# Optimization experiments

Measured on AMD Instinct MI355X. Metric: run time of the kernel, lower is better.

The kernel has to match this reference:

```python
import jax, jax.numpy as jnp
import numpy as np

N, V, E_PER = 8, 4608, 73728          # batch, nodes per graph, edges per graph
D_IN, C, NCLS = 1, 512, 3             # node feat dim, embed dim, classes
E = N * E_PER
LN_EPS = 1e-5


def setup_inputs() -> dict:
    key = jax.random.key(0)
    ks = jax.random.split(key, 12)
    x = jax.random.normal(ks[0], (N, 1, V, D_IN), jnp.float32)
    edge_index = jax.random.randint(ks[1], (2, E), 0, V, dtype=jnp.int32)
    edge_weight = jax.random.uniform(ks[2], (E,), jnp.float32)
    # GCNConv params: layer0 maps D_IN->C, layers 1..2 map C->C (weight [in,out], bias [out])
    w0 = jax.random.normal(ks[3], (D_IN, C), jnp.float32) * 0.02
    b0 = jnp.zeros((C,), jnp.float32)
    w1 = jax.random.normal(ks[4], (C, C), jnp.float32) * 0.02
    b1 = jnp.zeros((C,), jnp.float32)
    w2 = jax.random.normal(ks[5], (C, C), jnp.float32) * 0.02
    b2 = jnp.zeros((C,), jnp.float32)
    ln_g = jnp.ones((C,), jnp.float32)
    ln_b = jnp.zeros((C,), jnp.float32)
    head_w = jax.random.normal(ks[6], (C, NCLS), jnp.float32) * 2e-5
    head_b = jnp.log(jnp.full((NCLS,), 1.0 / NCLS, jnp.float32))
    return {"x": x, "edge_weight": edge_weight, "w0": w0, "b0": b0,
            "w1": w1, "b1": b1, "w2": w2, "b2": b2,
            "ln_g": ln_g, "ln_b": ln_b, "head_w": head_w, "head_b": head_b,
            "edge_index": edge_index}


def layer_norm(h, g, b):
    mu = h.mean(-1, keepdims=True)
    var = ((h - mu) ** 2).mean(-1, keepdims=True)
    return (h - mu) * jax.lax.rsqrt(var + LN_EPS) * g + b


def reference(x, edge_weight, w0, b0, w1, b1, w2, b2, ln_g, ln_b, head_w, head_b, edge_index):
    n, t, v, d = x.shape
    nv = n * v
    h = x.reshape(nv, d)
    # batch-offset local edge indices (edges are contiguous per graph)
    offs = jnp.repeat(jnp.arange(n, dtype=edge_index.dtype) * v, edge_index.shape[1] // n)
    src = edge_index[0] + offs
    tgt = edge_index[1] + offs
    # GCN norm with self-loops (fill weight 1.0), symmetric deg^-1/2 normalization
    loop = jnp.arange(nv, dtype=src.dtype)
    src_f = jnp.concatenate([src, loop])
    tgt_f = jnp.concatenate([tgt, loop])
    ew_f = jnp.concatenate([edge_weight, jnp.ones((nv,), edge_weight.dtype)])
    deg = jax.ops.segment_sum(ew_f, tgt_f, num_segments=nv)
    deg_safe = jnp.where(deg > 0, deg, 1.0)
    dinv = jnp.where(deg > 0, jax.lax.rsqrt(deg_safe), 0.0)
    norm = dinv[src_f] * ew_f * dinv[tgt_f]
    for w, bb in ((w0, b0), (w1, b1), (w2, b2)):
        hw = h @ w                                   # [NV, C]
        msg = norm[:, None] * hw[src_f]              # gather + scale  [E+NV, C]
        h = jax.ops.segment_sum(msg, tgt_f, num_segments=nv) + bb
        h = jax.nn.relu(h)
        h = layer_norm(h, ln_g, ln_b)
        # dropout is identity in eval mode
    pooled = h.reshape(n, v, -1).max(axis=1)         # global_max_pool (contiguous batch)
    pooled = layer_norm(pooled, ln_g, ln_b)
    return pooled @ head_w + head_b                  # [N, NCLS]
```

## Files before the change

### kernel.cpp

```cpp
#include <hip/hip_runtime.h>
#include <hip/hip_bf16.h>
#include <stdint.h>

#define N_GRAPH 8
#define V_NODES 4608
#define E_PER   73728
#define NV      (N_GRAPH * V_NODES)
#define E_TOT   (N_GRAPH * E_PER)
#define C       512
#define NCLS    3
#define LN_EPS  1e-5f
#define POOL_CHUNKS 36
#define SCAN_BLOCKS 144

typedef __attribute__((ext_vector_type(8))) short short8;
typedef __attribute__((ext_vector_type(4))) float floatx4;
typedef __attribute__((address_space(1))) void v_g;
typedef __attribute__((address_space(3))) void v_l;


__device__ inline float waveReduceSum(float v) {
#pragma unroll
    for (int o = 32; o > 0; o >>= 1) v += __shfl_down(v, o, 64);
    return v;
}

__device__ inline float waveAllSum(float v) {
#pragma unroll
    for (int o = 32; o > 0; o >>= 1) v += __shfl_xor(v, o, 64);
    return v;
}

__device__ inline float blockSum512(float v, volatile float* sred) {
    float s = waveReduceSum(v);
    if ((threadIdx.x & 63) == 0) sred[threadIdx.x >> 6] = s;
    __syncthreads();
    float t = 0.f;
#pragma unroll
    for (int i = 0; i < 8; i++) t += sred[i];
    __syncthreads();
    return t;
}

__device__ inline unsigned short f2bf(float f) {
    uint32_t u = __float_as_uint(f);
    u += 0x7fffu + ((u >> 16) & 1u);
    return (unsigned short)(u >> 16);
}
__device__ inline float bf2f(unsigned short b) {
    return __uint_as_float(((uint32_t)b) << 16);
}


__global__ void k_init(float* dinv, int* counts) {
    int i = blockIdx.x * 256 + threadIdx.x;
    if (i < NV) { dinv[i] = 1.0f; counts[i] = 0; }
}

__global__ void k_deg_count(const int* __restrict__ ei, const float* __restrict__ ew,
                            float* __restrict__ dinv, int* __restrict__ counts) {
    int e = blockIdx.x * 256 + threadIdx.x;
    if (e >= E_TOT) return;
    int off = (e / E_PER) * V_NODES;
    int t = ei[E_TOT + e] + off;
    atomicAdd(&dinv[t], ew[e]);
    atomicAdd(&counts[t], 1);
}

__global__ void k_rsqrt(float* dinv) {
    int i = blockIdx.x * 256 + threadIdx.x;
    if (i < NV) dinv[i] = rsqrtf(dinv[i]);
}


__global__ void k_scan1(const int* __restrict__ counts, int* __restrict__ row_ptr,
                        int* __restrict__ bsum) {
    __shared__ int sh[256];
    const int b = blockIdx.x, tid = threadIdx.x;
    const int idx = b * 256 + tid;
    int v = counts[idx];
    sh[tid] = v;
    __syncthreads();
#pragma unroll
    for (int off = 1; off < 256; off <<= 1) {
        int t = (tid >= off) ? sh[tid - off] : 0;
        __syncthreads();
        sh[tid] += t;
        __syncthreads();
    }
    row_ptr[idx] = sh[tid] - v;
    if (tid == 255) bsum[b] = sh[255];
}

__global__ void k_scan2(int* __restrict__ bsum) {
    __shared__ int sh[256];
    const int tid = threadIdx.x;
    int v = (tid < SCAN_BLOCKS) ? bsum[tid] : 0;
    sh[tid] = v;
    __syncthreads();
#pragma unroll
    for (int off = 1; off < 256; off <<= 1) {
        int t = (tid >= off) ? sh[tid - off] : 0;
        __syncthreads();
        sh[tid] += t;
        __syncthreads();
    }
    if (tid < SCAN_BLOCKS) bsum[tid] = sh[tid] - v;
}

__global__ void k_scan3(int* __restrict__ row_ptr, const int* __restrict__ bsum,
                        int* __restrict__ cursor) {
    const int b = blockIdx.x, tid = threadIdx.x;
    const int idx = b * 256 + tid;
    int v = row_ptr[idx] + bsum[b];
    row_ptr[idx] = v;
    cursor[idx] = v;
    if (idx == 0) row_ptr[NV] = E_TOT;
}

__global__ void k_fill(const int* __restrict__ ei, const float* __restrict__ ew,
                       const float* __restrict__ dinv, int* __restrict__ cursor,
                       int* __restrict__ col_idx, float* __restrict__ val) {
    int e = blockIdx.x * 256 + threadIdx.x;
    if (e >= E_TOT) return;
    int off = (e / E_PER) * V_NODES;
    int s = ei[e] + off;
    int t = ei[E_TOT + e] + off;
    int pos = atomicAdd(&cursor[t], 1);
    col_idx[pos] = s;
    val[pos] = dinv[s] * ew[e] * dinv[t];
}


__global__ void k_wt(const float* __restrict__ w1, const float* __restrict__ w2,
                     unsigned short* __restrict__ wt1, unsigned short* __restrict__ wt2) {
    int idx = blockIdx.x * 256 + threadIdx.x;
    int which = idx >> 18;
    int rem = idx & 0x3ffff;
    int n = rem >> 9, k = rem & 511;
    const float* W = which ? w2 : w1;
    unsigned short* WT = which ? wt2 : wt1;
    WT[n * C + k] = f2bf(W[k * C + n]);
}


__global__ void k_agg0_scalar(const float* __restrict__ x, const int* __restrict__ row_ptr,
                              const int* __restrict__ col_idx, const float* __restrict__ val,
                              const float* __restrict__ dinv, float* __restrict__ s0) {
    int t = blockIdx.x * 256 + threadIdx.x;
    if (t >= NV) return;
    float dt = dinv[t];
    float acc = dt * dt * x[t];
    int e1 = row_ptr[t + 1];
    for (int e = row_ptr[t]; e < e1; e++)
        acc += val[e] * x[col_idx[e]];
    s0[t] = acc;
}

__launch_bounds__(128)
__global__ void k_l0post(const float* __restrict__ s0, const float* __restrict__ w0,
                         const float* __restrict__ b0, const float* __restrict__ ln_g,
                         const float* __restrict__ ln_b, unsigned short* __restrict__ out) {
    const int t = blockIdx.x;
    const int tid = threadIdx.x;
    const int c4 = tid << 2;
    float s = s0[t];
    float4 w = *reinterpret_cast<const float4*>(&w0[c4]);
    float4 bb = *reinterpret_cast<const float4*>(&b0[c4]);
    float vx = fmaxf(s * w.x + bb.x, 0.f);
    float vy = fmaxf(s * w.y + bb.y, 0.f);
    float vz = fmaxf(s * w.z + bb.z, 0.f);
    float vw = fmaxf(s * w.w + bb.w, 0.f);
    __shared__ float redA[2], redB[2];
    float wsum = waveReduceSum(vx + vy + vz + vw);
    if ((tid & 63) == 0) redA[tid >> 6] = wsum;
    __syncthreads();
    float mu = (redA[0] + redA[1]) * (1.0f / C);
    float dx = vx - mu, dy = vy - mu, dz = vz - mu, dw = vw - mu;
    float wsq = waveReduceSum(dx * dx + dy * dy + dz * dz + dw * dw);
    if ((tid & 63) == 0) redB[tid >> 6] = wsq;
    __syncthreads();
    float rstd = rsqrtf((redB[0] + redB[1]) * (1.0f / C) + LN_EPS);
    float4 g = *reinterpret_cast<const float4*>(&ln_g[c4]);
    float4 b = *reinterpret_cast<const float4*>(&ln_b[c4]);
    ushort4 o = { f2bf(dx * rstd * g.x + b.x), f2bf(dy * rstd * g.y + b.y),
                  f2bf(dz * rstd * g.z + b.z), f2bf(dw * rstd * g.w + b.w) };
    reinterpret_cast<ushort4*>(out)[(size_t)t * 128 + tid] = o;
}


__launch_bounds__(256)
__global__ void k_gemm_mfma(const unsigned short* __restrict__ A,
                            const unsigned short* __restrict__ WT,
                            unsigned short* __restrict__ Bout) {
    __shared__ short8 lA[512];
    __shared__ short8 lB[512];
    const int tid = threadIdx.x;
    const int lane = tid & 63;
    const int wave = tid >> 6;
    const int wr = wave >> 1, wc = wave & 1;
    const int l15 = lane & 15, kg = lane >> 4;
    const int m0 = blockIdx.x * 128;
    const int n0 = blockIdx.y * 128;

    floatx4 acc[4][4] = {};

    const int s0i = tid, s1i = 256 + tid;
    const int kgs0 = s0i >> 7, idx0 = s0i & 127;
    const int kgs1 = s1i >> 7, idx1 = s1i & 127;
    const unsigned short* gA0 = A + (size_t)(m0 + idx0) * C + kgs0 * 8;
    const unsigned short* gA1 = A + (size_t)(m0 + idx1) * C + kgs1 * 8;
    const unsigned short* gB0 = WT + (size_t)(n0 + idx0) * C + kgs0 * 8;
    const unsigned short* gB1 = WT + (size_t)(n0 + idx1) * C + kgs1 * 8;

    for (int k0 = 0; k0 < C; k0 += 32) {
        __builtin_amdgcn_global_load_lds((v_g*)(gA0 + k0), (v_l*)&lA[s0i], 16, 0, 0);
        __builtin_amdgcn_global_load_lds((v_g*)(gA1 + k0), (v_l*)&lA[s1i], 16, 0, 0);
        __builtin_amdgcn_global_load_lds((v_g*)(gB0 + k0), (v_l*)&lB[s0i], 16, 0, 0);
        __builtin_amdgcn_global_load_lds((v_g*)(gB1 + k0), (v_l*)&lB[s1i], 16, 0, 0);
        asm volatile("s_waitcnt vmcnt(0)" ::: "memory");
        __syncthreads();

        short8 af[4], bf[4];
#pragma unroll
        for (int mi = 0; mi < 4; mi++)
            af[mi] = lA[kg * 128 + wr * 64 + mi * 16 + l15];
#pragma unroll
        for (int ni = 0; ni < 4; ni++)
            bf[ni] = lB[kg * 128 + wc * 64 + ni * 16 + l15];
#pragma unroll
        for (int mi = 0; mi < 4; mi++)
#pragma unroll
            for (int ni = 0; ni < 4; ni++)
                acc[mi][ni] = __builtin_amdgcn_mfma_f32_16x16x32_bf16(
                    af[mi], bf[ni], acc[mi][ni], 0, 0, 0);
        __syncthreads();
    }

#pragma unroll
    for (int mi = 0; mi < 4; mi++) {
#pragma unroll
        for (int ni = 0; ni < 4; ni++) {
            int n = n0 + wc * 64 + ni * 16 + l15;
#pragma unroll
            for (int r = 0; r < 4; r++) {
                int m = m0 + wr * 64 + mi * 16 + kg * 4 + r;
                Bout[(size_t)m * C + n] = f2bf(acc[mi][ni][r]);
            }
        }
    }
}


__launch_bounds__(256)
__global__ void k_agg(const unsigned short* __restrict__ hw, const int* __restrict__ row_ptr,
                      const int* __restrict__ col_idx, const float* __restrict__ val,
                      const float* __restrict__ dinv, const float* __restrict__ bias,
                      const float* __restrict__ ln_g, const float* __restrict__ ln_b,
                      unsigned short* __restrict__ out) {
    const int b = blockIdx.x;
    const int wv = threadIdx.x >> 6;
    const int lane = threadIdx.x & 63;
    const int t = (b & 7) * V_NODES + ((b >> 3) << 2) + wv;
    const int e0 = row_ptr[t], e1 = row_ptr[t + 1];
    const short8* hw8 = reinterpret_cast<const short8*>(hw);

    const float dt = dinv[t];
    const float selfw = dt * dt;
    short8 hs = hw8[(size_t)t * 64 + lane];
    float a[8];
#pragma unroll
    for (int i = 0; i < 8; i++) a[i] = selfw * bf2f((unsigned short)hs[i]);

    int e = e0;
    for (; e + 4 <= e1; e += 4) {
        int i0 = col_idx[e], i1 = col_idx[e + 1], i2 = col_idx[e + 2], i3 = col_idx[e + 3];
        float w0 = val[e], w1 = val[e + 1], w2 = val[e + 2], w3 = val[e + 3];
        short8 h0 = hw8[(size_t)i0 * 64 + lane];
        short8 h1 = hw8[(size_t)i1 * 64 + lane];
        short8 h2 = hw8[(size_t)i2 * 64 + lane];
        short8 h3 = hw8[(size_t)i3 * 64 + lane];
#pragma unroll
        for (int i = 0; i < 8; i++) a[i] += w0 * bf2f((unsigned short)h0[i]);
#pragma unroll
        for (int i = 0; i < 8; i++) a[i] += w1 * bf2f((unsigned short)h1[i]);
#pragma unroll
        for (int i = 0; i < 8; i++) a[i] += w2 * bf2f((unsigned short)h2[i]);
#pragma unroll
        for (int i = 0; i < 8; i++) a[i] += w3 * bf2f((unsigned short)h3[i]);
    }
    for (; e < e1; e++) {
        int is = col_idx[e];
        float w = val[e];
        short8 hv = hw8[(size_t)is * 64 + lane];
#pragma unroll
        for (int i = 0; i < 8; i++) a[i] += w * bf2f((unsigned short)hv[i]);
    }

    const int c8 = lane << 3;
    float4 bb0 = *reinterpret_cast<const float4*>(&bias[c8]);
    float4 bb1 = *reinterpret_cast<const float4*>(&bias[c8 + 4]);
    a[0] = fmaxf(a[0] + bb0.x, 0.f); a[1] = fmaxf(a[1] + bb0.y, 0.f);
    a[2] = fmaxf(a[2] + bb0.z, 0.f); a[3] = fmaxf(a[3] + bb0.w, 0.f);
    a[4] = fmaxf(a[4] + bb1.x, 0.f); a[5] = fmaxf(a[5] + bb1.y, 0.f);
    a[6] = fmaxf(a[6] + bb1.z, 0.f); a[7] = fmaxf(a[7] + bb1.w, 0.f);

    float s = a[0] + a[1] + a[2] + a[3] + a[4] + a[5] + a[6] + a[7];
    float mu = waveAllSum(s) * (1.0f / C);
    float sq = 0.f;
#pragma unroll
    for (int i = 0; i < 8; i++) { float d = a[i] - mu; sq += d * d; }
    float rstd = rsqrtf(waveAllSum(sq) * (1.0f / C) + LN_EPS);

    float4 g0 = *reinterpret_cast<const float4*>(&ln_g[c8]);
    float4 g1 = *reinterpret_cast<const float4*>(&ln_g[c8 + 4]);
    float4 z0 = *reinterpret_cast<const float4*>(&ln_b[c8]);
    float4 z1 = *reinterpret_cast<const float4*>(&ln_b[c8 + 4]);
    short8 o;
    o[0] = (short)f2bf((a[0] - mu) * rstd * g0.x + z0.x);
    o[1] = (short)f2bf((a[1] - mu) * rstd * g0.y + z0.y);
    o[2] = (short)f2bf((a[2] - mu) * rstd * g0.z + z0.z);
    o[3] = (short)f2bf((a[3] - mu) * rstd * g0.w + z0.w);
    o[4] = (short)f2bf((a[4] - mu) * rstd * g1.x + z1.x);
    o[5] = (short)f2bf((a[5] - mu) * rstd * g1.y + z1.y);
    o[6] = (short)f2bf((a[6] - mu) * rstd * g1.z + z1.z);
    o[7] = (short)f2bf((a[7] - mu) * rstd * g1.w + z1.w);
    reinterpret_cast<short8*>(out)[(size_t)t * 64 + lane] = o;
}


__global__ void k_pool1(const unsigned short* __restrict__ h, float* __restrict__ pmax) {
    int g = blockIdx.x, chunk = blockIdx.y;
    int c = threadIdx.x;
    int r0 = g * V_NODES + chunk * 128;
    float m = -1e30f;
#pragma unroll 4
    for (int r = 0; r < 128; r++)
        m = fmaxf(m, bf2f(h[(size_t)(r0 + r) * C + c]));
    pmax[((size_t)g * POOL_CHUNKS + chunk) * C + c] = m;
}

__global__ void k_pool2_head(const float* __restrict__ pmax, const float* __restrict__ ln_g,
                             const float* __restrict__ ln_b, const float* __restrict__ hw,
                             const float* __restrict__ hb, float* __restrict__ out) {
    __shared__ float sred[8];
    int g = blockIdx.x;
    int c = threadIdx.x;
    float m = -1e30f;
#pragma unroll
    for (int j = 0; j < POOL_CHUNKS; j++)
        m = fmaxf(m, pmax[((size_t)g * POOL_CHUNKS + j) * C + c]);
    float total = blockSum512(m, sred);
    float mu = total * (1.0f / C);
    float d = m - mu;
    float var = blockSum512(d * d, sred) * (1.0f / C);
    float rstd = rsqrtf(var + LN_EPS);
    float p = d * rstd * ln_g[c] + ln_b[c];
    float r0 = blockSum512(p * hw[c * NCLS + 0], sred);
    float r1 = blockSum512(p * hw[c * NCLS + 1], sred);
    float r2 = blockSum512(p * hw[c * NCLS + 2], sred);
    if (threadIdx.x == 0) {
        out[g * NCLS + 0] = r0 + hb[0];
        out[g * NCLS + 1] = r1 + hb[1];
        out[g * NCLS + 2] = r2 + hb[2];
    }
}


extern "C" void kernel_launch(void* const* d_in, const int* in_sizes, int n_in,
                              void* d_out, int out_size, void* d_ws, size_t ws_size,
                              hipStream_t stream) {
    const float* x      = (const float*)d_in[0];
    const float* ew     = (const float*)d_in[1];
    const float* w0     = (const float*)d_in[2];
    const float* b0     = (const float*)d_in[3];
    const float* w1     = (const float*)d_in[4];
    const float* b1     = (const float*)d_in[5];
    const float* w2     = (const float*)d_in[6];
    const float* b2     = (const float*)d_in[7];
    const float* ln_g   = (const float*)d_in[8];
    const float* ln_b   = (const float*)d_in[9];
    const float* head_w = (const float*)d_in[10];
    const float* head_b = (const float*)d_in[11];
    const int*   ei     = (const int*)d_in[12];
    float* out = (float*)d_out;

    char* p = (char*)d_ws;
    auto alloc = [&](size_t bytes) { void* r = p; p += (bytes + 255) & ~255ull; return r; };
    unsigned short* bufA = (unsigned short*)alloc((size_t)NV * C * 2);
    unsigned short* bufB = (unsigned short*)alloc((size_t)NV * C * 2);
    unsigned short* wt1  = (unsigned short*)alloc((size_t)C * C * 2);
    unsigned short* wt2  = (unsigned short*)alloc((size_t)C * C * 2);
    float* s0      = (float*)alloc((size_t)NV * 4);
    float* dinv    = (float*)alloc((size_t)NV * 4);
    int*   counts  = (int*)alloc((size_t)NV * 4);
    int*   row_ptr = (int*)alloc((size_t)(NV + 1) * 4);
    int*   cursor  = (int*)alloc((size_t)NV * 4);
    int*   bsum    = (int*)alloc((size_t)SCAN_BLOCKS * 4);
    int*   col_idx = (int*)alloc((size_t)E_TOT * 4);
    float* val     = (float*)alloc((size_t)E_TOT * 4);
    float* pmax    = (float*)alloc((size_t)N_GRAPH * POOL_CHUNKS * C * 4);

    k_init<<<NV / 256, 256, 0, stream>>>(dinv, counts);
    k_deg_count<<<E_TOT / 256, 256, 0, stream>>>(ei, ew, dinv, counts);
    k_rsqrt<<<NV / 256, 256, 0, stream>>>(dinv);
    k_scan1<<<SCAN_BLOCKS, 256, 0, stream>>>(counts, row_ptr, bsum);
    k_scan2<<<1, 256, 0, stream>>>(bsum);
    k_scan3<<<SCAN_BLOCKS, 256, 0, stream>>>(row_ptr, bsum, cursor);
    k_fill<<<E_TOT / 256, 256, 0, stream>>>(ei, ew, dinv, cursor, col_idx, val);
    k_wt<<<(2 * C * C) / 256, 256, 0, stream>>>(w1, w2, wt1, wt2);

    k_agg0_scalar<<<NV / 256, 256, 0, stream>>>(x, row_ptr, col_idx, val, dinv, s0);
    k_l0post<<<NV, 128, 0, stream>>>(s0, w0, b0, ln_g, ln_b, bufA);

    k_gemm_mfma<<<dim3(NV / 128, C / 128), 256, 0, stream>>>(bufA, wt1, bufB);
    k_agg<<<NV / 4, 256, 0, stream>>>(bufB, row_ptr, col_idx, val, dinv, b1, ln_g, ln_b, bufA);

    k_gemm_mfma<<<dim3(NV / 128, C / 128), 256, 0, stream>>>(bufA, wt2, bufB);
    k_agg<<<NV / 4, 256, 0, stream>>>(bufB, row_ptr, col_idx, val, dinv, b2, ln_g, ln_b, bufA);

    k_pool1<<<dim3(N_GRAPH, POOL_CHUNKS), C, 0, stream>>>(bufA, pmax);
    k_pool2_head<<<N_GRAPH, C, 0, stream>>>(pmax, ln_g, ln_b, head_w, head_b, out);
}
```

Measured before the change: 432.5 us.

## Build degree and CSR fill with per-block LDS atomics over node partitions

Replaces the global-atomic degree count (init, count and rsqrt kernels) with one kernel where each of 64 blocks owns a 576-node slice of one graph. It scans that graph's edges and accumulates degree and count with LDS atomics, then writes dinv and counts directly. The CSR fill also uses LDS cursors seeded from row_ptr, which removes the global cursor array and the global atomics. The trade-off is that each block reads all 73728 edges of its graph, so edge reads go up eightfold, and only 64 blocks run.

```diff
diff --git a/kernel.cpp b/kernel.cpp
--- a/kernel.cpp
+++ b/kernel.cpp
@@ -12,6 +12,7 @@
 #define LN_EPS  1e-5f
 #define POOL_CHUNKS 36
 #define SCAN_BLOCKS 144
+#define DPB     576
 
 typedef __attribute__((ext_vector_type(8))) short short8;
 typedef __attribute__((ext_vector_type(4))) float floatx4;
@@ -52,24 +53,32 @@
 }
 
 
-__global__ void k_init(float* dinv, int* counts) {
-    int i = blockIdx.x * 256 + threadIdx.x;
-    if (i < NV) { dinv[i] = 1.0f; counts[i] = 0; }
-}
-
-__global__ void k_deg_count(const int* __restrict__ ei, const float* __restrict__ ew,
-                            float* __restrict__ dinv, int* __restrict__ counts) {
-    int e = blockIdx.x * 256 + threadIdx.x;
-    if (e >= E_TOT) return;
-    int off = (e / E_PER) * V_NODES;
-    int t = ei[E_TOT + e] + off;
-    atomicAdd(&dinv[t], ew[e]);
-    atomicAdd(&counts[t], 1);
-}
-
-__global__ void k_rsqrt(float* dinv) {
-    int i = blockIdx.x * 256 + threadIdx.x;
-    if (i < NV) dinv[i] = rsqrtf(dinv[i]);
+__launch_bounds__(1024)
+__global__ void k_deg_lds(const int* __restrict__ ei, const float* __restrict__ ew,
+                          float* __restrict__ dinv, int* __restrict__ counts) {
+    __shared__ float degl[DPB];
+    __shared__ int   cntl[DPB];
+    const int b = blockIdx.x;
+    const int g = b >> 3, part = b & 7;
+    const int t0 = part * DPB;
+    const int tid = threadIdx.x;
+    for (int i = tid; i < DPB; i += 1024) { degl[i] = 1.0f; cntl[i] = 0; }
+    __syncthreads();
+    const int*   tgt = ei + E_TOT + g * E_PER;
+    const float* w   = ew + g * E_PER;
+    for (int e = tid; e < E_PER; e += 1024) {
+        int tl = tgt[e] - t0;
+        if ((unsigned)tl < DPB) {
+            atomicAdd(&degl[tl], w[e]);
+            atomicAdd(&cntl[tl], 1);
+        }
+    }
+    __syncthreads();
+    for (int i = tid; i < DPB; i += 1024) {
+        int node = g * V_NODES + t0 + i;
+        dinv[node]   = rsqrtf(degl[i]);
+        counts[node] = cntl[i];
+    }
 }
 
 
@@ -108,27 +117,37 @@
     if (tid < SCAN_BLOCKS) bsum[tid] = sh[tid] - v;
 }
 
-__global__ void k_scan3(int* __restrict__ row_ptr, const int* __restrict__ bsum,
-                        int* __restrict__ cursor) {
+__global__ void k_scan3(int* __restrict__ row_ptr, const int* __restrict__ bsum) {
     const int b = blockIdx.x, tid = threadIdx.x;
     const int idx = b * 256 + tid;
-    int v = row_ptr[idx] + bsum[b];
-    row_ptr[idx] = v;
-    cursor[idx] = v;
+    row_ptr[idx] += bsum[b];
     if (idx == 0) row_ptr[NV] = E_TOT;
 }
 
-__global__ void k_fill(const int* __restrict__ ei, const float* __restrict__ ew,
-                       const float* __restrict__ dinv, int* __restrict__ cursor,
-                       int* __restrict__ col_idx, float* __restrict__ val) {
-    int e = blockIdx.x * 256 + threadIdx.x;
-    if (e >= E_TOT) return;
-    int off = (e / E_PER) * V_NODES;
-    int s = ei[e] + off;
-    int t = ei[E_TOT + e] + off;
-    int pos = atomicAdd(&cursor[t], 1);
-    col_idx[pos] = s;
-    val[pos] = dinv[s] * ew[e] * dinv[t];
+__launch_bounds__(1024)
+__global__ void k_fill_lds(const int* __restrict__ ei, const float* __restrict__ ew,
+                           const float* __restrict__ dinv, const int* __restrict__ row_ptr,
+                           int* __restrict__ col_idx, float* __restrict__ val) {
+    __shared__ int curl[DPB];
+    const int b = blockIdx.x;
+    const int g = b >> 3, part = b & 7;
+    const int t0 = part * DPB;
+    const int nbase = g * V_NODES + t0;
+    const int tid = threadIdx.x;
+    for (int i = tid; i < DPB; i += 1024) curl[i] = row_ptr[nbase + i];
+    __syncthreads();
+    const int*   src = ei + g * E_PER;
+    const int*   tgt = ei + E_TOT + g * E_PER;
+    const float* w   = ew + g * E_PER;
+    for (int e = tid; e < E_PER; e += 1024) {
+        int tl = tgt[e] - t0;
+        if ((unsigned)tl < DPB) {
+            int s = src[e] + g * V_NODES;
+            int pos = atomicAdd(&curl[tl], 1);
+            col_idx[pos] = s;
+            val[pos] = dinv[s] * w[e] * dinv[nbase + tl];
+        }
+    }
 }
 
 
@@ -395,19 +414,16 @@
     float* dinv    = (float*)alloc((size_t)NV * 4);
     int*   counts  = (int*)alloc((size_t)NV * 4);
     int*   row_ptr = (int*)alloc((size_t)(NV + 1) * 4);
-    int*   cursor  = (int*)alloc((size_t)NV * 4);
     int*   bsum    = (int*)alloc((size_t)SCAN_BLOCKS * 4);
     int*   col_idx = (int*)alloc((size_t)E_TOT * 4);
     float* val     = (float*)alloc((size_t)E_TOT * 4);
     float* pmax    = (float*)alloc((size_t)N_GRAPH * POOL_CHUNKS * C * 4);
 
-    k_init<<<NV / 256, 256, 0, stream>>>(dinv, counts);
-    k_deg_count<<<E_TOT / 256, 256, 0, stream>>>(ei, ew, dinv, counts);
-    k_rsqrt<<<NV / 256, 256, 0, stream>>>(dinv);
+    k_deg_lds<<<64, 1024, 0, stream>>>(ei, ew, dinv, counts);
     k_scan1<<<SCAN_BLOCKS, 256, 0, stream>>>(counts, row_ptr, bsum);
     k_scan2<<<1, 256, 0, stream>>>(bsum);
-    k_scan3<<<SCAN_BLOCKS, 256, 0, stream>>>(row_ptr, bsum, cursor);
-    k_fill<<<E_TOT / 256, 256, 0, stream>>>(ei, ew, dinv, cursor, col_idx, val);
+    k_scan3<<<SCAN_BLOCKS, 256, 0, stream>>>(row_ptr, bsum);
+    k_fill_lds<<<64, 1024, 0, stream>>>(ei, ew, dinv, row_ptr, col_idx, val);
     k_wt<<<(2 * C * C) / 256, 256, 0, stream>>>(w1, w2, wt1, wt2);
 
     k_agg0_scalar<<<NV / 256, 256, 0, stream>>>(x, row_ptr, col_idx, val, dinv, s0);
```

Result: slower. 452.6 us (+4.7%).
